# Optimization experiments

Measured on AMD Instinct MI355X. Metric: run time of the kernel, lower is better.

Reference implementation:

```python
import jax, jax.numpy as jnp
import numpy as np

N, D = 2048, 64
H, W = 128, 128
NEAR, RADIUS_CLIP, BLUR = 0.01, 3.0, 0.3
A_MIN, A_MAX = 1.0 / 255.0, 0.999


def setup_inputs():
    key = jax.random.key(0)
    k = jax.random.split(key, 6)
    xy = jax.random.uniform(k[0], (N, 2), minval=-1.2, maxval=1.2)
    zz = jax.random.uniform(k[1], (N, 1), minval=3.0, maxval=5.0)
    means = jnp.concatenate([xy, zz], axis=1).astype(jnp.float32)
    quats = jax.random.normal(k[2], (N, 4), dtype=jnp.float32)
    scales = jax.random.normal(k[3], (N, 3), dtype=jnp.float32) * 0.3 - 2.2  # log-scales
    opacities = jax.random.normal(k[4], (N,), dtype=jnp.float32) * 0.5 + 1.0  # logits
    gs_features = jax.random.normal(k[5], (N, D), dtype=jnp.float32) * 0.5
    c2o = jnp.eye(4, dtype=jnp.float32)
    K = jnp.array([[200.0, 0.0, 64.0], [0.0, 200.0, 64.0], [0.0, 0.0, 1.0]], dtype=jnp.float32)
    return dict(means=means, quats=quats, scales=scales, opacities=opacities,
                gs_features=gs_features, c2o=c2o, K=K, width=W, height=H)


def _quat_to_rot(q):
    q = q / jnp.linalg.norm(q, axis=-1, keepdims=True)
    w, x, y, z = q[:, 0], q[:, 1], q[:, 2], q[:, 3]
    r0 = jnp.stack([1 - 2 * (y * y + z * z), 2 * (x * y - w * z), 2 * (x * z + w * y)], -1)
    r1 = jnp.stack([2 * (x * y + w * z), 1 - 2 * (x * x + z * z), 2 * (y * z - w * x)], -1)
    r2 = jnp.stack([2 * (x * z - w * y), 2 * (y * z + w * x), 1 - 2 * (x * x + y * y)], -1)
    return jnp.stack([r0, r1, r2], -2)  # [N,3,3]


def _rasterize(means, quats, log_scales, opac_logits, colors, viewmat, K, width, height):
    Rv, tv = viewmat[:3, :3], viewmat[:3, 3]
    fx, fy, cx, cy = K[0, 0], K[1, 1], K[0, 2], K[1, 2]
    mc = means @ Rv.T + tv                      # camera-space means [N,3]
    x, y, z = mc[:, 0], mc[:, 1], mc[:, 2]
    # 3D covariance Sigma = R S S^T R^T, rotated into camera frame
    M = _quat_to_rot(quats) * jnp.exp(log_scales)[:, None, :]
    cov_w = M @ jnp.swapaxes(M, 1, 2)           # [N,3,3]
    cov_c = jnp.einsum('ij,njk,lk->nil', Rv, cov_w, Rv)
    # perspective (EWA) Jacobian [N,2,3]
    rz = 1.0 / z
    zero = jnp.zeros_like(z)
    J = jnp.stack([jnp.stack([fx * rz, zero, -fx * x * rz * rz], -1),
                   jnp.stack([zero, fy * rz, -fy * y * rz * rz], -1)], -2)
    cov2d = jnp.einsum('nij,njk,nlk->nil', J, cov_c, J)
    a = cov2d[:, 0, 0] + BLUR
    b = cov2d[:, 0, 1]
    c = cov2d[:, 1, 1] + BLUR
    det = a * c - b * b
    cA, cB, cC = c / det, -b / det, a / det     # conic = inverse 2D covariance
    mx = fx * x * rz + cx
    my = fy * y * rz + cy
    # cull: behind near plane, degenerate, or projected 3-sigma radius below radius_clip
    lam_max = 0.5 * (a + c) + jnp.sqrt(jnp.maximum(0.25 * (a - c) ** 2 + b * b, 1e-12))
    radius = 3.0 * jnp.sqrt(lam_max)
    valid = (z > NEAR) & (det > 0) & (radius > RADIUS_CLIP)
    opac = jax.nn.sigmoid(opac_logits)
    # global front-to-back depth order (single camera)
    order = jnp.argsort(z)
    mx, my, cA, cB, cC = mx[order], my[order], cA[order], cB[order], cC[order]
    opac, valid, colors = opac[order], valid[order], colors[order]
    # per pixel-gaussian evaluation, [H,W,N]
    px = jnp.arange(width, dtype=means.dtype) + 0.5
    py = jnp.arange(height, dtype=means.dtype) + 0.5
    dx = px[None, :, None] - mx[None, None, :]
    dy = py[:, None, None] - my[None, None, :]
    sigma = 0.5 * (cA * dx * dx + cC * dy * dy) + cB * dx * dy
    alpha = jnp.minimum(opac * jnp.exp(-sigma), A_MAX)
    alpha = jnp.where((sigma >= 0) & valid & (alpha >= A_MIN), alpha, 0.0)
    # front-to-back alpha compositing: exclusive transmittance cumprod
    Tcum = jnp.cumprod(1.0 - alpha, axis=-1)
    T_excl = jnp.concatenate([jnp.ones_like(Tcum[..., :1]), Tcum[..., :-1]], axis=-1)
    out = jnp.einsum('hwn,nd->hwd', alpha * T_excl, colors)
    return out[None]  # [1,H,W,D]


def reference(means, quats, scales, opacities, gs_features, c2o, K, width, height):
    viewmat = jnp.linalg.inv(c2o)
    return _rasterize(means, quats, scales, opacities, gs_features, viewmat, K, width, height)
```

## Files before the change

kernel.cpp:

```cpp
#include <hip/hip_runtime.h>

constexpr int NG = 2048;
constexpr int DF = 64;
constexpr int IW = 128;
constexpr int IH = 128;
constexpr int SEG = 8;
constexpr int SEGN = NG / SEG;
constexpr int RB = SEG * 64;
constexpr int JC = 8;
constexpr int JCN = NG / JC;

#define P_NEAR 0.01f
#define P_BLUR 0.3f
#define P_AMIN (1.0f/255.0f)
#define P_AMAX 0.999f

constexpr int L_LIST = 0;
constexpr int L_T    = SEG * SEGN;
constexpr int L_ACC  = L_T + SEG * 64;
constexpr int ACC_STRIDE = 66;
constexpr int L_TOTAL = L_ACC + SEG * 64 * ACC_STRIDE;

__device__ inline void invert4x4(const float* m, float* inv) {
    inv[0]  =  m[5]*m[10]*m[15] - m[5]*m[11]*m[14] - m[9]*m[6]*m[15] + m[9]*m[7]*m[14] + m[13]*m[6]*m[11] - m[13]*m[7]*m[10];
    inv[4]  = -m[4]*m[10]*m[15] + m[4]*m[11]*m[14] + m[8]*m[6]*m[15] - m[8]*m[7]*m[14] - m[12]*m[6]*m[11] + m[12]*m[7]*m[10];
    inv[8]  =  m[4]*m[9]*m[15]  - m[4]*m[11]*m[13] - m[8]*m[5]*m[15] + m[8]*m[7]*m[13] + m[12]*m[5]*m[11] - m[12]*m[7]*m[9];
    inv[12] = -m[4]*m[9]*m[14]  + m[4]*m[10]*m[13] + m[8]*m[5]*m[14] - m[8]*m[6]*m[13] - m[12]*m[5]*m[10] + m[12]*m[6]*m[9];
    inv[1]  = -m[1]*m[10]*m[15] + m[1]*m[11]*m[14] + m[9]*m[2]*m[15] - m[9]*m[3]*m[14] - m[13]*m[2]*m[11] + m[13]*m[3]*m[10];
    inv[5]  =  m[0]*m[10]*m[15] - m[0]*m[11]*m[14] - m[8]*m[2]*m[15] + m[8]*m[3]*m[14] + m[12]*m[2]*m[11] - m[12]*m[3]*m[10];
    inv[9]  = -m[0]*m[9]*m[15]  + m[0]*m[11]*m[13] + m[8]*m[1]*m[15] - m[8]*m[3]*m[13] - m[12]*m[1]*m[11] + m[12]*m[3]*m[9];
    inv[13] =  m[0]*m[9]*m[14]  - m[0]*m[10]*m[13] - m[8]*m[1]*m[14] + m[8]*m[2]*m[13] + m[12]*m[1]*m[10] - m[12]*m[2]*m[9];
    inv[2]  =  m[1]*m[6]*m[15]  - m[1]*m[7]*m[14]  - m[5]*m[2]*m[15] + m[5]*m[3]*m[14] + m[13]*m[2]*m[7]  - m[13]*m[3]*m[6];
    inv[6]  = -m[0]*m[6]*m[15]  + m[0]*m[7]*m[14]  + m[4]*m[2]*m[15] - m[4]*m[3]*m[14] - m[12]*m[2]*m[7]  + m[12]*m[3]*m[6];
    inv[10] =  m[0]*m[5]*m[15]  - m[0]*m[7]*m[13]  - m[4]*m[1]*m[15] + m[4]*m[3]*m[13] + m[12]*m[1]*m[7]  - m[12]*m[3]*m[5];
    inv[14] = -m[0]*m[5]*m[14]  + m[0]*m[6]*m[13]  + m[4]*m[1]*m[14] - m[4]*m[2]*m[13] - m[12]*m[1]*m[6]  + m[12]*m[2]*m[5];
    inv[3]  = -m[1]*m[6]*m[11]  + m[1]*m[7]*m[10]  + m[5]*m[2]*m[11] - m[5]*m[3]*m[10] - m[9]*m[2]*m[7]   + m[9]*m[3]*m[6];
    inv[7]  =  m[0]*m[6]*m[11]  - m[0]*m[7]*m[10]  - m[4]*m[2]*m[11] + m[4]*m[3]*m[10] + m[8]*m[2]*m[7]   - m[8]*m[3]*m[6];
    inv[11] = -m[0]*m[5]*m[11]  + m[0]*m[7]*m[9]   + m[4]*m[1]*m[11] - m[4]*m[3]*m[9]  - m[8]*m[1]*m[7]   + m[8]*m[3]*m[5];
    inv[15] =  m[0]*m[5]*m[10]  - m[0]*m[6]*m[9]   - m[4]*m[1]*m[10] + m[4]*m[2]*m[9]  + m[8]*m[1]*m[6]   - m[8]*m[2]*m[5];
    float det = m[0]*inv[0] + m[1]*inv[4] + m[2]*inv[8] + m[3]*inv[12];
    det = 1.0f / det;
    #pragma unroll
    for (int i = 0; i < 16; ++i) inv[i] *= det;
}

__global__ __launch_bounds__(256) void preprocess_kernel(
    const float* __restrict__ means,  const float* __restrict__ quats,
    const float* __restrict__ scales, const float* __restrict__ opac_logits,
    const float* __restrict__ c2o,    const float* __restrict__ Kmat,
    float* __restrict__ zkey, float* __restrict__ evalp, float* __restrict__ bboxp)
{
    const int i = blockIdx.x * 256 + threadIdx.x;
    if (i >= NG) return;

    float inv[16];
    {
        float m[16];
        #pragma unroll
        for (int t = 0; t < 16; ++t) m[t] = c2o[t];
        invert4x4(m, inv);
    }
    const float fx = Kmat[0], fy = Kmat[4], cx = Kmat[2], cy = Kmat[5];

    float mx = means[i*3+0], my = means[i*3+1], mz = means[i*3+2];
    float X = inv[0]*mx + inv[1]*my + inv[2]*mz  + inv[3];
    float Y = inv[4]*mx + inv[5]*my + inv[6]*mz  + inv[7];
    float Z = inv[8]*mx + inv[9]*my + inv[10]*mz + inv[11];

    float qw = quats[i*4+0], qx = quats[i*4+1], qy = quats[i*4+2], qz = quats[i*4+3];
    float qn = rsqrtf(qw*qw + qx*qx + qy*qy + qz*qz);
    qw *= qn; qx *= qn; qy *= qn; qz *= qn;
    float R00 = 1.f - 2.f*(qy*qy + qz*qz), R01 = 2.f*(qx*qy - qw*qz), R02 = 2.f*(qx*qz + qw*qy);
    float R10 = 2.f*(qx*qy + qw*qz), R11 = 1.f - 2.f*(qx*qx + qz*qz), R12 = 2.f*(qy*qz - qw*qx);
    float R20 = 2.f*(qx*qz - qw*qy), R21 = 2.f*(qy*qz + qw*qx), R22 = 1.f - 2.f*(qx*qx + qy*qy);

    float s0 = expf(scales[i*3+0]), s1 = expf(scales[i*3+1]), s2 = expf(scales[i*3+2]);
    float M00 = R00*s0, M01 = R01*s1, M02 = R02*s2;
    float M10 = R10*s0, M11 = R11*s1, M12 = R12*s2;
    float M20 = R20*s0, M21 = R21*s1, M22 = R22*s2;

    float V[3][3];
    V[0][0] = M00*M00 + M01*M01 + M02*M02;
    V[0][1] = M00*M10 + M01*M11 + M02*M12;
    V[0][2] = M00*M20 + M01*M21 + M02*M22;
    V[1][1] = M10*M10 + M11*M11 + M12*M12;
    V[1][2] = M10*M20 + M11*M21 + M12*M22;
    V[2][2] = M20*M20 + M21*M21 + M22*M22;
    V[1][0] = V[0][1]; V[2][0] = V[0][2]; V[2][1] = V[1][2];

    float Rv[3][3] = {{inv[0],inv[1],inv[2]},{inv[4],inv[5],inv[6]},{inv[8],inv[9],inv[10]}};
    float Tm[3][3], C[3][3];
    #pragma unroll
    for (int r = 0; r < 3; ++r)
        #pragma unroll
        for (int c = 0; c < 3; ++c)
            Tm[r][c] = Rv[r][0]*V[0][c] + Rv[r][1]*V[1][c] + Rv[r][2]*V[2][c];
    #pragma unroll
    for (int r = 0; r < 3; ++r)
        #pragma unroll
        for (int c = 0; c < 3; ++c)
            C[r][c] = Tm[r][0]*Rv[c][0] + Tm[r][1]*Rv[c][1] + Tm[r][2]*Rv[c][2];

    float rz = 1.0f / Z;
    float j00 = fx*rz, j02 = -fx*X*rz*rz;
    float j11 = fy*rz, j12 = -fy*Y*rz*rz;

    float c00 = j00*j00*C[0][0] + 2.f*j00*j02*C[0][2] + j02*j02*C[2][2];
    float c01 = j00*j11*C[0][1] + j00*j12*C[0][2] + j02*j11*C[1][2] + j02*j12*C[2][2];
    float c11 = j11*j11*C[1][1] + 2.f*j11*j12*C[1][2] + j12*j12*C[2][2];

    float a = c00 + P_BLUR;
    float b = c01;
    float c = c11 + P_BLUR;
    float det = a*c - b*b;

    float pmx = fx*X*rz + cx;
    float pmy = fy*Y*rz + cy;

    float lam = 0.5f*(a + c) + sqrtf(fmaxf(0.25f*(a - c)*(a - c) + b*b, 1e-12f));
    float radius = 3.0f * sqrtf(lam);
    bool valid = (Z > P_NEAR) && (det > 0.0f) && (radius > 3.0f);

    float op = 1.0f / (1.0f + expf(-opac_logits[i]));

    float cA = 0.f, cB = 0.f, cC = 0.f, rx = -1e9f, ry = -1e9f;
    if (valid) {
        float rdet = 1.0f / det;
        cA = c * rdet; cB = -b * rdet; cC = a * rdet;
        float smax = logf(255.0f * op);
        if (smax > 0.f) {
            rx = sqrtf(2.f * a * smax) * 1.0001f + 1e-3f;
            ry = sqrtf(2.f * c * smax) * 1.0001f + 1e-3f;
        }
    } else {
        op = 0.f;
    }

    zkey[i] = Z;
    ((float4*)evalp)[i*2]   = make_float4(pmx, pmy, cA, cB);
    ((float4*)evalp)[i*2+1] = make_float4(cC, op, 0.f, 0.f);
    ((float4*)bboxp)[i]     = make_float4(pmx, pmy, rx, ry);
}

__global__ __launch_bounds__(256) void rank_partial_kernel(
    const float* __restrict__ zkey, int* __restrict__ partial)
{
    __shared__ float zj[JCN];
    const int ib = blockIdx.x & 7;
    const int jc = blockIdx.x >> 3;
    const int tid = threadIdx.x;
    const int i = ib * 256 + tid;

    zj[tid] = zkey[jc * JCN + tid];
    __syncthreads();

    const float zi = zkey[i];
    const int jbase = jc * JCN;
    const float4* z4 = (const float4*)zj;
    int cnt = 0;
    #pragma unroll 8
    for (int c = 0; c < JCN/4; ++c) {
        float4 z = z4[c];
        int j = jbase + 4*c;
        cnt += (z.x < zi) || (z.x == zi && (j+0) < i);
        cnt += (z.y < zi) || (z.y == zi && (j+1) < i);
        cnt += (z.z < zi) || (z.z == zi && (j+2) < i);
        cnt += (z.w < zi) || (z.w == zi && (j+3) < i);
    }
    partial[jc * NG + i] = cnt;
}

__global__ __launch_bounds__(256) void permute_kernel(
    const int* __restrict__ partial, const float* __restrict__ evalp,
    const float* __restrict__ bboxp, float* __restrict__ evalps,
    float* __restrict__ bboxs)
{
    const int i = blockIdx.x * 256 + threadIdx.x;
    if (i >= NG) return;
    int rank = 0;
    #pragma unroll
    for (int c = 0; c < JC; ++c) rank += partial[c * NG + i];

    float4 lo = ((const float4*)evalp)[i*2];
    float4 hi = ((const float4*)evalp)[i*2+1];
    hi.z = __int_as_float(i);
    ((float4*)evalps)[rank*2]   = lo;
    ((float4*)evalps)[rank*2+1] = hi;
    ((float4*)bboxs)[rank]      = ((const float4*)bboxp)[i];
}

__global__ __launch_bounds__(RB, 2) void render_kernel(
    const float* __restrict__ evalps, const float* __restrict__ bboxs,
    const float* __restrict__ colors, float* __restrict__ out)
{
    extern __shared__ float lds[];
    const int tid  = threadIdx.x;
    const int lane = tid & 63;
    const int seg  = tid >> 6;
    const int tile = blockIdx.x;
    const int tx = (tile & 15) * 8;
    const int ty = (tile >> 4) * 8;
    const float px = tx + (lane & 7) + 0.5f;
    const float py = ty + (lane >> 3) + 0.5f;
    const float cxt = tx + 4.0f, cyt = ty + 4.0f;

    int* list = (int*)(lds + L_LIST) + seg * SEGN;
    int cnt = 0;
    const float4* bb4 = (const float4*)bboxs;
    for (int c = 0; c < SEGN; c += 64) {
        int g = seg * SEGN + c + lane;
        float4 bb = bb4[g];
        bool sel = (fabsf(bb.x - cxt) <= bb.z + 3.5f) &&
                   (fabsf(bb.y - cyt) <= bb.w + 3.5f);
        unsigned long long m = __ballot(sel);
        if (sel) list[cnt + (int)__popcll(m & ((1ull << lane) - 1ull))] = g;
        cnt += (int)__popcll(m);
    }

    float acc[64];
    #pragma unroll
    for (int f = 0; f < 64; ++f) acc[f] = 0.f;
    float T = 1.0f;

    const float4* ep4 = (const float4*)evalps;
    const float4* cp4 = (const float4*)colors;

    if (cnt > 0) {
        int gi = list[0];
        float4 e0 = ep4[gi*2], e1 = ep4[gi*2+1];
        for (int r = 0; r < cnt; ++r) {
            int gin = (r + 1 < cnt) ? list[r + 1] : gi;
            float4 n0 = ep4[gin*2], n1 = ep4[gin*2+1];

            float dx = px - e0.x, dy = py - e0.y;
            float sig = 0.5f*(e0.z*dx*dx + e1.x*dy*dy) + e0.w*dx*dy;
            float al = fminf(e1.y * __expf(-sig), P_AMAX);
            al = (sig >= 0.f && al >= P_AMIN) ? al : 0.f;

            if (__ballot(al > 0.f)) {
                float wv = T * al;
                const float4* crow = cp4 + (size_t)(unsigned)__float_as_int(e1.z) * 16;
                #pragma unroll
                for (int q = 0; q < 16; ++q) {
                    float4 cv = crow[q];
                    acc[4*q+0] = fmaf(wv, cv.x, acc[4*q+0]);
                    acc[4*q+1] = fmaf(wv, cv.y, acc[4*q+1]);
                    acc[4*q+2] = fmaf(wv, cv.z, acc[4*q+2]);
                    acc[4*q+3] = fmaf(wv, cv.w, acc[4*q+3]);
                }
                T *= (1.f - al);
                if (!__ballot(T >= 1e-6f)) break;
            }
            e0 = n0; e1 = n1;
        }
    }

    {
        float* ab = lds + L_ACC + (size_t)(seg * 64 + lane) * ACC_STRIDE;
        #pragma unroll
        for (int q = 0; q < 32; ++q)
            *(float2*)(ab + 2*q) = make_float2(acc[2*q], acc[2*q+1]);
        lds[L_T + seg*64 + lane] = T;
    }
    __syncthreads();

    {
        int p  = tid >> 3;
        int f0 = (tid & 7) * 8;
        float r[8];
        const float* ab = lds + L_ACC + (size_t)((SEG-1)*64 + p) * ACC_STRIDE + f0;
        #pragma unroll
        for (int j = 0; j < 4; ++j) {
            float2 u = *(const float2*)(ab + 2*j);
            r[2*j] = u.x; r[2*j+1] = u.y;
        }
        #pragma unroll
        for (int s = SEG - 2; s >= 0; --s) {
            float Ts = lds[L_T + s*64 + p];
            const float* as_ = lds + L_ACC + (size_t)(s*64 + p) * ACC_STRIDE + f0;
            #pragma unroll
            for (int j = 0; j < 4; ++j) {
                float2 u = *(const float2*)(as_ + 2*j);
                r[2*j]   = fmaf(Ts, r[2*j],   u.x);
                r[2*j+1] = fmaf(Ts, r[2*j+1], u.y);
            }
        }
        int pyg = ty + (p >> 3), pxg = tx + (p & 7);
        float* op_ = out + (size_t)(pyg * IW + pxg) * DF + f0;
        *(float4*)op_       = make_float4(r[0], r[1], r[2], r[3]);
        *(float4*)(op_ + 4) = make_float4(r[4], r[5], r[6], r[7]);
    }
}

extern "C" void kernel_launch(void* const* d_in, const int* in_sizes, int n_in,
                              void* d_out, int out_size, void* d_ws, size_t ws_size,
                              hipStream_t stream) {
    const float* means  = (const float*)d_in[0];
    const float* quats  = (const float*)d_in[1];
    const float* scales = (const float*)d_in[2];
    const float* opac   = (const float*)d_in[3];
    const float* colors = (const float*)d_in[4];
    const float* c2o    = (const float*)d_in[5];
    const float* Kmat   = (const float*)d_in[6];
    float* out = (float*)d_out;

    float* ws     = (float*)d_ws;
    float* zkey   = ws;
    float* evalp  = ws + NG;
    float* bboxp  = ws + NG*9;
    float* evalps = ws + NG*13;
    float* bboxs  = ws + NG*21;
    int*   partial= (int*)(ws + NG*25);

    (void)hipFuncSetAttribute((const void*)render_kernel,
                              hipFuncAttributeMaxDynamicSharedMemorySize,
                              L_TOTAL * 4);

    preprocess_kernel<<<NG/256, 256, 0, stream>>>(means, quats, scales, opac, c2o, Kmat,
                                                  zkey, evalp, bboxp);
    rank_partial_kernel<<<8 * JC, 256, 0, stream>>>(zkey, partial);
    permute_kernel<<<NG/256, 256, 0, stream>>>(partial, evalp, bboxp, evalps, bboxs);
    render_kernel<<<IH*IW/64, RB, L_TOTAL*4, stream>>>(evalps, bboxs, colors, out);
}
```

Baseline: 123.8 us.

## Fuse preprocessing, sorting and rendering into one per-tile kernel

Replaces the four-kernel pipeline (preprocess, global rank, permute, render) with a single kernel. Each 8x8 tile block recomputes projection for all gaussians, culls them to its tile into LDS, rank-sorts the survivors locally by depth key, and splits the sorted list across the 8 segments for compositing. This removes three launches and the global workspace round-trips, but every tile block now redoes preprocessing for all 2048 gaussians. The per-tile list is capped at 1024 entries, so a tile with more overlapping gaussians silently drops the extras.

```diff
diff --git a/kernel.cpp b/kernel.cpp
--- a/kernel.cpp
+++ b/kernel.cpp
@@ -1,23 +1,24 @@
 #include <hip/hip_runtime.h>
 
-constexpr int NG = 2048;
-constexpr int DF = 64;
-constexpr int IW = 128;
-constexpr int IH = 128;
+constexpr int NG  = 2048;
+constexpr int DF  = 64;
+constexpr int IW  = 128;
+constexpr int IH  = 128;
 constexpr int SEG = 8;
-constexpr int SEGN = NG / SEG;
-constexpr int RB = SEG * 64;
-constexpr int JC = 8;
-constexpr int JCN = NG / JC;
+constexpr int RB  = SEG * 64;
+constexpr int CAP = 1024;
 
 #define P_NEAR 0.01f
 #define P_BLUR 0.3f
 #define P_AMIN (1.0f/255.0f)
 #define P_AMAX 0.999f
 
-constexpr int L_LIST = 0;
-constexpr int L_T    = SEG * SEGN;
-constexpr int L_ACC  = L_T + SEG * 64;
+constexpr int L_T    = 0;
+constexpr int L_CNT  = 512;
+constexpr int L_SIDX = 528;
+constexpr int L_ACC  = L_SIDX + CAP;
+constexpr int L_PRM  = L_ACC;
+constexpr int L_KEYS = L_PRM + CAP * 8;
 constexpr int ACC_STRIDE = 66;
 constexpr int L_TOTAL = L_ACC + SEG * 64 * ACC_STRIDE;
 
@@ -44,156 +45,18 @@
     for (int i = 0; i < 16; ++i) inv[i] *= det;
 }
 
-__global__ __launch_bounds__(256) void preprocess_kernel(
+__global__ __launch_bounds__(RB) void fused_render_kernel(
     const float* __restrict__ means,  const float* __restrict__ quats,
     const float* __restrict__ scales, const float* __restrict__ opac_logits,
-    const float* __restrict__ c2o,    const float* __restrict__ Kmat,
-    float* __restrict__ zkey, float* __restrict__ evalp, float* __restrict__ bboxp)
-{
-    const int i = blockIdx.x * 256 + threadIdx.x;
-    if (i >= NG) return;
-
-    float inv[16];
-    {
-        float m[16];
-        #pragma unroll
-        for (int t = 0; t < 16; ++t) m[t] = c2o[t];
-        invert4x4(m, inv);
-    }
-    const float fx = Kmat[0], fy = Kmat[4], cx = Kmat[2], cy = Kmat[5];
-
-    float mx = means[i*3+0], my = means[i*3+1], mz = means[i*3+2];
-    float X = inv[0]*mx + inv[1]*my + inv[2]*mz  + inv[3];
-    float Y = inv[4]*mx + inv[5]*my + inv[6]*mz  + inv[7];
-    float Z = inv[8]*mx + inv[9]*my + inv[10]*mz + inv[11];
-
-    float qw = quats[i*4+0], qx = quats[i*4+1], qy = quats[i*4+2], qz = quats[i*4+3];
-    float qn = rsqrtf(qw*qw + qx*qx + qy*qy + qz*qz);
-    qw *= qn; qx *= qn; qy *= qn; qz *= qn;
-    float R00 = 1.f - 2.f*(qy*qy + qz*qz), R01 = 2.f*(qx*qy - qw*qz), R02 = 2.f*(qx*qz + qw*qy);
-    float R10 = 2.f*(qx*qy + qw*qz), R11 = 1.f - 2.f*(qx*qx + qz*qz), R12 = 2.f*(qy*qz - qw*qx);
-    float R20 = 2.f*(qx*qz - qw*qy), R21 = 2.f*(qy*qz + qw*qx), R22 = 1.f - 2.f*(qx*qx + qy*qy);
-
-    float s0 = expf(scales[i*3+0]), s1 = expf(scales[i*3+1]), s2 = expf(scales[i*3+2]);
-    float M00 = R00*s0, M01 = R01*s1, M02 = R02*s2;
-    float M10 = R10*s0, M11 = R11*s1, M12 = R12*s2;
-    float M20 = R20*s0, M21 = R21*s1, M22 = R22*s2;
-
-    float V[3][3];
-    V[0][0] = M00*M00 + M01*M01 + M02*M02;
-    V[0][1] = M00*M10 + M01*M11 + M02*M12;
-    V[0][2] = M00*M20 + M01*M21 + M02*M22;
-    V[1][1] = M10*M10 + M11*M11 + M12*M12;
-    V[1][2] = M10*M20 + M11*M21 + M12*M22;
-    V[2][2] = M20*M20 + M21*M21 + M22*M22;
-    V[1][0] = V[0][1]; V[2][0] = V[0][2]; V[2][1] = V[1][2];
-
-    float Rv[3][3] = {{inv[0],inv[1],inv[2]},{inv[4],inv[5],inv[6]},{inv[8],inv[9],inv[10]}};
-    float Tm[3][3], C[3][3];
-    #pragma unroll
-    for (int r = 0; r < 3; ++r)
-        #pragma unroll
-        for (int c = 0; c < 3; ++c)
-            Tm[r][c] = Rv[r][0]*V[0][c] + Rv[r][1]*V[1][c] + Rv[r][2]*V[2][c];
-    #pragma unroll
-    for (int r = 0; r < 3; ++r)
-        #pragma unroll
-        for (int c = 0; c < 3; ++c)
-            C[r][c] = Tm[r][0]*Rv[c][0] + Tm[r][1]*Rv[c][1] + Tm[r][2]*Rv[c][2];
-
-    float rz = 1.0f / Z;
-    float j00 = fx*rz, j02 = -fx*X*rz*rz;
-    float j11 = fy*rz, j12 = -fy*Y*rz*rz;
-
-    float c00 = j00*j00*C[0][0] + 2.f*j00*j02*C[0][2] + j02*j02*C[2][2];
-    float c01 = j00*j11*C[0][1] + j00*j12*C[0][2] + j02*j11*C[1][2] + j02*j12*C[2][2];
-    float c11 = j11*j11*C[1][1] + 2.f*j11*j12*C[1][2] + j12*j12*C[2][2];
-
-    float a = c00 + P_BLUR;
-    float b = c01;
-    float c = c11 + P_BLUR;
-    float det = a*c - b*b;
-
-    float pmx = fx*X*rz + cx;
-    float pmy = fy*Y*rz + cy;
-
-    float lam = 0.5f*(a + c) + sqrtf(fmaxf(0.25f*(a - c)*(a - c) + b*b, 1e-12f));
-    float radius = 3.0f * sqrtf(lam);
-    bool valid = (Z > P_NEAR) && (det > 0.0f) && (radius > 3.0f);
-
-    float op = 1.0f / (1.0f + expf(-opac_logits[i]));
-
-    float cA = 0.f, cB = 0.f, cC = 0.f, rx = -1e9f, ry = -1e9f;
-    if (valid) {
-        float rdet = 1.0f / det;
-        cA = c * rdet; cB = -b * rdet; cC = a * rdet;
-        float smax = logf(255.0f * op);
-        if (smax > 0.f) {
-            rx = sqrtf(2.f * a * smax) * 1.0001f + 1e-3f;
-            ry = sqrtf(2.f * c * smax) * 1.0001f + 1e-3f;
-        }
-    } else {
-        op = 0.f;
-    }
-
-    zkey[i] = Z;
-    ((float4*)evalp)[i*2]   = make_float4(pmx, pmy, cA, cB);
-    ((float4*)evalp)[i*2+1] = make_float4(cC, op, 0.f, 0.f);
-    ((float4*)bboxp)[i]     = make_float4(pmx, pmy, rx, ry);
-}
-
-__global__ __launch_bounds__(256) void rank_partial_kernel(
-    const float* __restrict__ zkey, int* __restrict__ partial)
-{
-    __shared__ float zj[JCN];
-    const int ib = blockIdx.x & 7;
-    const int jc = blockIdx.x >> 3;
-    const int tid = threadIdx.x;
-    const int i = ib * 256 + tid;
-
-    zj[tid] = zkey[jc * JCN + tid];
-    __syncthreads();
-
-    const float zi = zkey[i];
-    const int jbase = jc * JCN;
-    const float4* z4 = (const float4*)zj;
-    int cnt = 0;
-    #pragma unroll 8
-    for (int c = 0; c < JCN/4; ++c) {
-        float4 z = z4[c];
-        int j = jbase + 4*c;
-        cnt += (z.x < zi) || (z.x == zi && (j+0) < i);
-        cnt += (z.y < zi) || (z.y == zi && (j+1) < i);
-        cnt += (z.z < zi) || (z.z == zi && (j+2) < i);
-        cnt += (z.w < zi) || (z.w == zi && (j+3) < i);
-    }
-    partial[jc * NG + i] = cnt;
-}
-
-__global__ __launch_bounds__(256) void permute_kernel(
-    const int* __restrict__ partial, const float* __restrict__ evalp,
-    const float* __restrict__ bboxp, float* __restrict__ evalps,
-    float* __restrict__ bboxs)
-{
-    const int i = blockIdx.x * 256 + threadIdx.x;
-    if (i >= NG) return;
-    int rank = 0;
-    #pragma unroll
-    for (int c = 0; c < JC; ++c) rank += partial[c * NG + i];
-
-    float4 lo = ((const float4*)evalp)[i*2];
-    float4 hi = ((const float4*)evalp)[i*2+1];
-    hi.z = __int_as_float(i);
-    ((float4*)evalps)[rank*2]   = lo;
-    ((float4*)evalps)[rank*2+1] = hi;
-    ((float4*)bboxs)[rank]      = ((const float4*)bboxp)[i];
-}
-
-__global__ __launch_bounds__(RB, 2) void render_kernel(
-    const float* __restrict__ evalps, const float* __restrict__ bboxs,
-    const float* __restrict__ colors, float* __restrict__ out)
+    const float* __restrict__ colors, const float* __restrict__ c2o,
+    const float* __restrict__ Kmat,   float* __restrict__ out)
 {
     extern __shared__ float lds[];
+    int*                cnt  = (int*)(lds + L_CNT);
+    int*                sidx = (int*)(lds + L_SIDX);
+    unsigned long long* keys = (unsigned long long*)(lds + L_KEYS);
+    float4*             prm4 = (float4*)(lds + L_PRM);
+
     const int tid  = threadIdx.x;
     const int lane = tid & 63;
     const int seg  = tid >> 6;
@@ -204,57 +67,174 @@
     const float py = ty + (lane >> 3) + 0.5f;
     const float cxt = tx + 4.0f, cyt = ty + 4.0f;
 
-    int* list = (int*)(lds + L_LIST) + seg * SEGN;
-    int cnt = 0;
-    const float4* bb4 = (const float4*)bboxs;
-    for (int c = 0; c < SEGN; c += 64) {
-        int g = seg * SEGN + c + lane;
-        float4 bb = bb4[g];
-        bool sel = (fabsf(bb.x - cxt) <= bb.z + 3.5f) &&
-                   (fabsf(bb.y - cyt) <= bb.w + 3.5f);
-        unsigned long long m = __ballot(sel);
-        if (sel) list[cnt + (int)__popcll(m & ((1ull << lane) - 1ull))] = g;
-        cnt += (int)__popcll(m);
-    }
+    if (tid == 0) *cnt = 0;
+    __syncthreads();
+
+    {
+        float inv[16];
+        {
+            float m[16];
+            #pragma unroll
+            for (int t = 0; t < 16; ++t) m[t] = c2o[t];
+            invert4x4(m, inv);
+        }
+        const float fx = Kmat[0], fy = Kmat[4], cx = Kmat[2], cy = Kmat[5];
+
+        for (int c = 0; c < NG / RB; ++c) {
+            const int g = c * RB + tid;
+            float mx = means[g*3+0], my = means[g*3+1], mz = means[g*3+2];
+            float X = inv[0]*mx + inv[1]*my + inv[2]*mz  + inv[3];
+            float Y = inv[4]*mx + inv[5]*my + inv[6]*mz  + inv[7];
+            float Z = inv[8]*mx + inv[9]*my + inv[10]*mz + inv[11];
+
+            float qw = quats[g*4+0], qx = quats[g*4+1], qy = quats[g*4+2], qz = quats[g*4+3];
+            float qn = rsqrtf(qw*qw + qx*qx + qy*qy + qz*qz);
+            qw *= qn; qx *= qn; qy *= qn; qz *= qn;
+            float R00 = 1.f - 2.f*(qy*qy + qz*qz), R01 = 2.f*(qx*qy - qw*qz), R02 = 2.f*(qx*qz + qw*qy);
+            float R10 = 2.f*(qx*qy + qw*qz), R11 = 1.f - 2.f*(qx*qx + qz*qz), R12 = 2.f*(qy*qz - qw*qx);
+            float R20 = 2.f*(qx*qz - qw*qy), R21 = 2.f*(qy*qz + qw*qx), R22 = 1.f - 2.f*(qx*qx + qy*qy);
+
+            float s0 = expf(scales[g*3+0]), s1 = expf(scales[g*3+1]), s2 = expf(scales[g*3+2]);
+            float M00 = R00*s0, M01 = R01*s1, M02 = R02*s2;
+            float M10 = R10*s0, M11 = R11*s1, M12 = R12*s2;
+            float M20 = R20*s0, M21 = R21*s1, M22 = R22*s2;
+
+            float V00 = M00*M00 + M01*M01 + M02*M02;
+            float V01 = M00*M10 + M01*M11 + M02*M12;
+            float V02 = M00*M20 + M01*M21 + M02*M22;
+            float V11 = M10*M10 + M11*M11 + M12*M12;
+            float V12 = M10*M20 + M11*M21 + M12*M22;
+            float V22 = M20*M20 + M21*M21 + M22*M22;
+
+            float Rv[3][3] = {{inv[0],inv[1],inv[2]},{inv[4],inv[5],inv[6]},{inv[8],inv[9],inv[10]}};
+            float Vm[3][3] = {{V00,V01,V02},{V01,V11,V12},{V02,V12,V22}};
+            float Tm[3][3], C[3][3];
+            #pragma unroll
+            for (int r = 0; r < 3; ++r)
+                #pragma unroll
+                for (int cc = 0; cc < 3; ++cc)
+                    Tm[r][cc] = Rv[r][0]*Vm[0][cc] + Rv[r][1]*Vm[1][cc] + Rv[r][2]*Vm[2][cc];
+            #pragma unroll
+            for (int r = 0; r < 3; ++r)
+                #pragma unroll
+                for (int cc = 0; cc < 3; ++cc)
+                    C[r][cc] = Tm[r][0]*Rv[cc][0] + Tm[r][1]*Rv[cc][1] + Tm[r][2]*Rv[cc][2];
+
+            float rz = 1.0f / Z;
+            float j00 = fx*rz, j02 = -fx*X*rz*rz;
+            float j11 = fy*rz, j12 = -fy*Y*rz*rz;
+
+            float c00 = j00*j00*C[0][0] + 2.f*j00*j02*C[0][2] + j02*j02*C[2][2];
+            float c01 = j00*j11*C[0][1] + j00*j12*C[0][2] + j02*j11*C[1][2] + j02*j12*C[2][2];
+            float c11 = j11*j11*C[1][1] + 2.f*j11*j12*C[1][2] + j12*j12*C[2][2];
+
+            float a = c00 + P_BLUR;
+            float b = c01;
+            float cc_ = c11 + P_BLUR;
+            float det = a*cc_ - b*b;
+
+            float pmx = fx*X*rz + cx;
+            float pmy = fy*Y*rz + cy;
+
+            float lam = 0.5f*(a + cc_) + sqrtf(fmaxf(0.25f*(a - cc_)*(a - cc_) + b*b, 1e-12f));
+            float radius = 3.0f * sqrtf(lam);
+            bool valid = (Z > P_NEAR) && (det > 0.0f) && (radius > 3.0f);
+
+            float op = 1.0f / (1.0f + expf(-opac_logits[g]));
+
+            bool sel = false;
+            float cA = 0.f, cB = 0.f, cC2 = 0.f;
+            if (valid) {
+                float rdet = 1.0f / det;
+                cA = cc_ * rdet; cB = -b * rdet; cC2 = a * rdet;
+                float smax = logf(255.0f * op);
+                if (smax > 0.f) {
+                    float rx = sqrtf(2.f * a   * smax) * 1.0001f + 1e-3f;
+                    float ry = sqrtf(2.f * cc_ * smax) * 1.0001f + 1e-3f;
+                    sel = (fabsf(pmx - cxt) <= rx + 3.5f) && (fabsf(pmy - cyt) <= ry + 3.5f);
+                }
+            }
+
+            unsigned long long m = __ballot(sel);
+            int wbase = 0;
+            if (lane == 0 && m) wbase = atomicAdd(cnt, (int)__popcll(m));
+            wbase = __shfl(wbase, 0);
+            if (sel) {
+                int pos = wbase + (int)__popcll(m & ((1ull << lane) - 1ull));
+                if (pos < CAP) {
+                    prm4[pos*2]   = make_float4(pmx, pmy, cA, cB);
+                    prm4[pos*2+1] = make_float4(cC2, op, __int_as_float(g), 0.f);
+                    keys[pos] = ((unsigned long long)__float_as_uint(Z) << 32) | (unsigned)g;
+                }
+            }
+        }
+    }
+    __syncthreads();
+    int L = *cnt;
+    if (L > CAP) L = CAP;
+
+    {
+        int padL = (L + 1) & ~1;
+        if (tid < padL - L) keys[L + tid] = ~0ull;
+        __syncthreads();
+        const ulonglong2* k2 = (const ulonglong2*)keys;
+        for (int k = tid; k < L; k += RB) {
+            unsigned long long kk = keys[k];
+            int rank = 0;
+            #pragma unroll 2
+            for (int c = 0; c < padL / 2; ++c) {
+                ulonglong2 q = k2[c];
+                rank += (q.x < kk) + (q.y < kk);
+            }
+            sidx[rank] = k;
+        }
+    }
+    __syncthreads();
 
     float acc[64];
     #pragma unroll
     for (int f = 0; f < 64; ++f) acc[f] = 0.f;
     float T = 1.0f;
 
-    const float4* ep4 = (const float4*)evalps;
-    const float4* cp4 = (const float4*)colors;
-
-    if (cnt > 0) {
-        int gi = list[0];
-        float4 e0 = ep4[gi*2], e1 = ep4[gi*2+1];
-        for (int r = 0; r < cnt; ++r) {
-            int gin = (r + 1 < cnt) ? list[r + 1] : gi;
-            float4 n0 = ep4[gin*2], n1 = ep4[gin*2+1];
-
-            float dx = px - e0.x, dy = py - e0.y;
-            float sig = 0.5f*(e0.z*dx*dx + e1.x*dy*dy) + e0.w*dx*dy;
-            float al = fminf(e1.y * __expf(-sig), P_AMAX);
-            al = (sig >= 0.f && al >= P_AMIN) ? al : 0.f;
-
-            if (__ballot(al > 0.f)) {
-                float wv = T * al;
+    {
+        const int r0 = (seg * L) >> 3;
+        const int r1 = ((seg + 1) * L) >> 3;
+        const float4* cp4 = (const float4*)colors;
+        if (r1 > r0) {
+            int k = sidx[r0];
+            float4 e0 = prm4[k*2], e1 = prm4[k*2+1];
+            for (int r = r0; r < r1; ++r) {
+                int kn = (r + 1 < r1) ? sidx[r + 1] : k;
+                float4 f0 = prm4[kn*2], f1 = prm4[kn*2+1];
+
                 const float4* crow = cp4 + (size_t)(unsigned)__float_as_int(e1.z) * 16;
+                float4 cbuf[16];
                 #pragma unroll
-                for (int q = 0; q < 16; ++q) {
-                    float4 cv = crow[q];
-                    acc[4*q+0] = fmaf(wv, cv.x, acc[4*q+0]);
-                    acc[4*q+1] = fmaf(wv, cv.y, acc[4*q+1]);
-                    acc[4*q+2] = fmaf(wv, cv.z, acc[4*q+2]);
-                    acc[4*q+3] = fmaf(wv, cv.w, acc[4*q+3]);
+                for (int q = 0; q < 16; ++q) cbuf[q] = crow[q];
+
+                float dx = px - e0.x, dy = py - e0.y;
+                float sig = 0.5f*(e0.z*dx*dx + e1.x*dy*dy) + e0.w*dx*dy;
+                float al = fminf(e1.y * __expf(-sig), P_AMAX);
+                al = (sig >= 0.f && al >= P_AMIN) ? al : 0.f;
+
+                if (__ballot(al > 0.f)) {
+                    float wv = T * al;
+                    #pragma unroll
+                    for (int q = 0; q < 16; ++q) {
+                        acc[4*q+0] = fmaf(wv, cbuf[q].x, acc[4*q+0]);
+                        acc[4*q+1] = fmaf(wv, cbuf[q].y, acc[4*q+1]);
+                        acc[4*q+2] = fmaf(wv, cbuf[q].z, acc[4*q+2]);
+                        acc[4*q+3] = fmaf(wv, cbuf[q].w, acc[4*q+3]);
+                    }
+                    T *= (1.f - al);
+                    if (!__ballot(T >= 1e-6f)) break;
                 }
-                T *= (1.f - al);
-                if (!__ballot(T >= 1e-6f)) break;
-            }
-            e0 = n0; e1 = n1;
-        }
-    }
-
+                e0 = f0; e1 = f1; k = kn;
+            }
+        }
+    }
+
+    __syncthreads();
     {
         float* ab = lds + L_ACC + (size_t)(seg * 64 + lane) * ACC_STRIDE;
         #pragma unroll
@@ -303,22 +283,12 @@
     const float* c2o    = (const float*)d_in[5];
     const float* Kmat   = (const float*)d_in[6];
     float* out = (float*)d_out;
-
-    float* ws     = (float*)d_ws;
-    float* zkey   = ws;
-    float* evalp  = ws + NG;
-    float* bboxp  = ws + NG*9;
-    float* evalps = ws + NG*13;
-    float* bboxs  = ws + NG*21;
-    int*   partial= (int*)(ws + NG*25);
-
-    (void)hipFuncSetAttribute((const void*)render_kernel,
+    (void)d_ws; (void)ws_size;
+
+    (void)hipFuncSetAttribute((const void*)fused_render_kernel,
                               hipFuncAttributeMaxDynamicSharedMemorySize,
                               L_TOTAL * 4);
 
-    preprocess_kernel<<<NG/256, 256, 0, stream>>>(means, quats, scales, opac, c2o, Kmat,
-                                                  zkey, evalp, bboxp);
-    rank_partial_kernel<<<8 * JC, 256, 0, stream>>>(zkey, partial);
-    permute_kernel<<<NG/256, 256, 0, stream>>>(partial, evalp, bboxp, evalps, bboxs);
-    render_kernel<<<IH*IW/64, RB, L_TOTAL*4, stream>>>(evalps, bboxs, colors, out);
+    fused_render_kernel<<<IH*IW/64, RB, L_TOTAL*4, stream>>>(
+        means, quats, scales, opac, colors, c2o, Kmat, out);
 }
```

New measurement: 118.7 us. -4.1%, faster.
